# Optimization experiments

Measured on AMD Instinct MI355X. Metric: run time of the kernel, lower is better.

## Reference

```python
import jax, jax.numpy as jnp
import numpy as np

N = 100000   # nodes
E = 1600000  # edges (before self loops)
D = 128      # input_dim
H1 = 128     # hidden_dim_1
H2 = 128     # hidden_dim_2
OUT = 1      # output_dim
G = 64       # number of graphs in the batch


def setup_inputs() -> dict:
    key = jax.random.key(0)
    ks = jax.random.split(key, 11)
    x = jax.random.normal(ks[0], (N, D), dtype=jnp.float32)
    edge_index = jax.random.randint(ks[1], (2, E), 0, N, dtype=jnp.int64)
    batch = jnp.sort(jax.random.randint(ks[2], (N,), 0, G, dtype=jnp.int64))
    s = 0.05
    W1 = jax.random.normal(ks[3], (D, H1), dtype=jnp.float32) * s
    b1 = jnp.zeros((H1,), dtype=jnp.float32)
    W2 = jax.random.normal(ks[4], (H1, H2), dtype=jnp.float32) * s
    b2 = jnp.zeros((H2,), dtype=jnp.float32)
    W_iou = jax.random.normal(ks[5], (H2, OUT), dtype=jnp.float32) * s
    b_iou = jnp.zeros((OUT,), dtype=jnp.float32)
    W_iop = jax.random.normal(ks[6], (H2, OUT), dtype=jnp.float32) * s
    b_iop = jnp.zeros((OUT,), dtype=jnp.float32)
    return dict(x=x, edge_index=edge_index, batch=batch,
                W1=W1, b1=b1, W2=W2, b2=b2,
                W_iou=W_iou, b_iou=b_iou, W_iop=W_iop, b_iop=b_iop)


def reference(x, edge_index, batch, W1, b1, W2, b2, W_iou, b_iou, W_iop, b_iop):
    n = x.shape[0]
    # add_self_loops
    loops = jnp.arange(n, dtype=edge_index.dtype)
    src = jnp.concatenate([edge_index[0], loops])
    dst = jnp.concatenate([edge_index[1], loops])
    # symmetric GCN normalization: deg over target nodes
    deg = jax.ops.segment_sum(jnp.ones_like(dst, dtype=x.dtype), dst, num_segments=n)
    dinv = jnp.where(deg > 0, jax.lax.rsqrt(deg), 0.0)
    norm = dinv[src] * dinv[dst]  # [E+N]

    def gcn_conv(h, W, b):
        hw = h @ W                                  # [N, H]
        m = hw[src] * norm[:, None]                 # gather + normalize [E+N, H]
        return jax.ops.segment_sum(m, dst, num_segments=n) + b  # scatter-add

    h = jax.nn.relu(gcn_conv(x, W1, b1))
    h = jax.nn.relu(gcn_conv(h, W2, b2))
    # global_max_pool over graph ids
    pooled = jax.ops.segment_max(h, batch, num_segments=G)
    pooled = jnp.where(jnp.isfinite(pooled), pooled, 0.0)  # guard empty graphs
    iou = pooled @ W_iou + b_iou
    iop = pooled @ W_iop + b_iop
    return jnp.concatenate([iou, iop], axis=1)  # [G, 2*OUT]
```

## Files before the change

### kernel.cpp

```cpp
#include <hip/hip_runtime.h>
#include <math.h>

typedef unsigned int u32;
typedef __attribute__((ext_vector_type(8))) short short8v;
typedef __attribute__((ext_vector_type(4))) float floatx4;

__device__ inline int rfl(int v) { return __builtin_amdgcn_readfirstlane(v); }

__device__ inline float blo(u32 u) { return __uint_as_float(u << 16); }
__device__ inline float bhi(u32 u) { return __uint_as_float(u & 0xffff0000u); }
__device__ inline u32 f2b(float f) {
    u32 u = __float_as_uint(f);
    return (u + 0x7fffu + ((u >> 16) & 1u)) >> 16;
}
__device__ inline u32 pack2(float a, float b) { return f2b(a) | (f2b(b) << 16); }

__global__ void init_k(u32* gcursor, int B, int CAP, u32* pooled, int np) {
    int i = blockIdx.x * blockDim.x + threadIdx.x;
    if (i < np) pooled[i] = 0u;
    if (i < B) gcursor[i] = (u32)i * (u32)CAP;
}

__global__ __launch_bounds__(256) void wprep_k(const float* __restrict__ W1, const float* __restrict__ W2,
                                               ushort* __restrict__ W1t, ushort* __restrict__ W2t) {
    int idx = blockIdx.x * 256 + threadIdx.x;
    int k = idx >> 7, j = idx & 127;
    W1t[j * 128 + k] = (ushort)f2b(W1[idx]);
    W2t[j * 128 + k] = (ushort)f2b(W2[idx]);
}

#define FILL_EPT 16
__global__ __launch_bounds__(256) void bfill_k(const int* __restrict__ src, const int* __restrict__ dst,
                                               u32* __restrict__ gcursor, u32* __restrict__ pairs,
                                               int E, int B, int CAP) {
    __shared__ u32 lcnt[256];
    __shared__ u32 lbase[256];
    const int t = threadIdx.x;
    lcnt[t] = 0;
    __syncthreads();

    const int base_e = blockIdx.x * (256 * FILL_EPT);
    u32 pk[FILL_EPT];
    u32 bk[FILL_EPT];
    u32 rk[FILL_EPT];
#pragma unroll
    for (int j = 0; j < FILL_EPT; ++j) {
        int e = base_e + t + j * 256;
        pk[j] = 0xFFFFFFFFu;
        if (e < E) {
            int d = dst[e];
            int s = src[e];
            u32 b = (u32)d >> 9;
            pk[j] = (u32)s | (((u32)d & 511u) << 17);
            bk[j] = b;
            rk[j] = atomicAdd(&lcnt[b], 1u);
        }
    }
    __syncthreads();
    if (t < B) {
        u32 v = lcnt[t];
        lbase[t] = v ? atomicAdd(&gcursor[t], v) : 0u;
    }
    __syncthreads();
#pragma unroll
    for (int j = 0; j < FILL_EPT; ++j) {
        if (pk[j] != 0xFFFFFFFFu) {
            u32 b = bk[j];
            u32 pos = lbase[b] + rk[j];
            if (pos < (b + 1u) * (u32)CAP) pairs[pos] = pk[j];
        }
    }
}

__global__ __launch_bounds__(256) void csort_k(const u32* __restrict__ pairs, const u32* __restrict__ gcursor,
                                               u32* __restrict__ csr, uint2* __restrict__ rowinfo,
                                               float* __restrict__ dinv, int N, int CAP) {
    __shared__ u32 hist[512];
    __shared__ u32 excl[512];
    __shared__ u32 pscan[256];
    const int b = blockIdx.x, t = threadIdx.x;
    const u32 base = (u32)b * (u32)CAP;
    u32 cnt = gcursor[b] - base;
    if (cnt > (u32)CAP) cnt = (u32)CAP;

    hist[t] = 0u; hist[t + 256] = 0u;
    __syncthreads();
    for (u32 j = t; j < cnt; j += 256) {
        u32 p = pairs[base + j];
        atomicAdd(&hist[p >> 17], 1u);
    }
    __syncthreads();
    u32 a = hist[2 * t], c = hist[2 * t + 1];
    u32 s = a + c;
    pscan[t] = s;
    __syncthreads();
    for (int off = 1; off < 256; off <<= 1) {
        u32 v = (t >= off) ? pscan[t - off] : 0u;
        __syncthreads();
        pscan[t] += v;
        __syncthreads();
    }
    u32 e0 = pscan[t] - s;
    excl[2 * t] = e0;
    excl[2 * t + 1] = e0 + a;
    __syncthreads();
    const int node0 = b << 9;
#pragma unroll
    for (int q = 0; q < 2; ++q) {
        int loc = t + q * 256;
        int i = node0 + loc;
        if (i < N) {
            u32 dg = hist[loc];
            rowinfo[i] = make_uint2(base + excl[loc], dg);
            dinv[i] = rsqrtf((float)(dg + 1u));
        }
    }
    __syncthreads();
    for (u32 j = t; j < cnt; j += 256) {
        u32 p = pairs[base + j];
        u32 loc = p >> 17;
        u32 pos = atomicAdd(&excl[loc], 1u);
        csr[base + pos] = p & 0x1FFFFu;
    }
}

__device__ inline int swz(int row, int kbyte) { return row * 256 + (kbyte ^ ((row & 7) << 4)); }

template <bool BF16IN>
__global__ __launch_bounds__(256) void gemm_mfma_k(const void* __restrict__ inp, const ushort* __restrict__ Wt,
                                                   const float* __restrict__ dinv,
                                                   ushort* __restrict__ outp, int N) {
    __shared__ char Xl[128 * 256];
    __shared__ char Wl[128 * 256];
    const int t = threadIdx.x;
    const int brow = blockIdx.x * 128;

    {
        const uint4* g = (const uint4*)Wt;
#pragma unroll
        for (int i = 0; i < 8; ++i) {
            int f = t + i * 256;
            int r = f >> 4, kb = (f & 15) << 4;
            *(uint4*)(Wl + swz(r, kb)) = g[f];
        }
    }
    if (BF16IN) {
#pragma unroll
        for (int i = 0; i < 8; ++i) {
            int f = t + i * 256;
            int r = f >> 4, kb = (f & 15) << 4;
            int gr = brow + r;
            uint4 v = make_uint4(0u, 0u, 0u, 0u);
            if (gr < N) v = ((const uint4*)inp)[gr * 16 + (kb >> 4)];
            *(uint4*)(Xl + swz(r, kb)) = v;
        }
    } else {
#pragma unroll
        for (int i = 0; i < 16; ++i) {
            int f = t + i * 256;
            int r = f >> 5, c4 = (f & 31) << 2;
            int gr = brow + r;
            uint2 v = make_uint2(0u, 0u);
            if (gr < N) {
                float4 x = ((const float4*)inp)[gr * 32 + (c4 >> 2)];
                v.x = pack2(x.x, x.y);
                v.y = pack2(x.z, x.w);
            }
            *(uint2*)(Xl + swz(r, c4 * 2)) = v;
        }
    }
    __syncthreads();

    const int lane = t & 63;
    const int wave = t >> 6;
    const int l15 = lane & 15;
    const int lk = (lane >> 4) * 16;

    floatx4 acc[2][8];
#pragma unroll
    for (int mt = 0; mt < 2; ++mt)
#pragma unroll
        for (int nt = 0; nt < 8; ++nt) acc[mt][nt] = (floatx4){0.f, 0.f, 0.f, 0.f};

#pragma unroll
    for (int ks = 0; ks < 4; ++ks) {
        int kb = ks * 64 + lk;
        short8v a[2], b[8];
#pragma unroll
        for (int mt = 0; mt < 2; ++mt) {
            int row = wave * 32 + mt * 16 + l15;
            a[mt] = *(const short8v*)(Xl + swz(row, kb));
        }
#pragma unroll
        for (int nt = 0; nt < 8; ++nt) {
            int jr = nt * 16 + l15;
            b[nt] = *(const short8v*)(Wl + swz(jr, kb));
        }
#pragma unroll
        for (int mt = 0; mt < 2; ++mt)
#pragma unroll
            for (int nt = 0; nt < 8; ++nt)
                acc[mt][nt] = __builtin_amdgcn_mfma_f32_16x16x32_bf16(a[mt], b[nt], acc[mt][nt], 0, 0, 0);
    }

    const int r0w = (lane >> 4) * 4;
#pragma unroll
    for (int mt = 0; mt < 2; ++mt) {
#pragma unroll
        for (int reg = 0; reg < 4; ++reg) {
            int grow = brow + wave * 32 + mt * 16 + r0w + reg;
            if (grow < N) {
                float sc = dinv[grow];
#pragma unroll
                for (int nt = 0; nt < 8; ++nt)
                    outp[grow * 128 + nt * 16 + l15] = (ushort)f2b(acc[mt][nt][reg] * sc);
            }
        }
    }
}

__global__ __launch_bounds__(256) void edge_accum_k(const u32* __restrict__ hw, const uint2* __restrict__ rowinfo,
                                                    const u32* __restrict__ csr, const float* __restrict__ dinv,
                                                    const float* __restrict__ bias, u32* __restrict__ hout, int N) {
    const int lane = threadIdx.x & 63;
    const int wid = (blockIdx.x * blockDim.x + threadIdx.x) >> 6;
    const int nw = (gridDim.x * blockDim.x) >> 6;
    const float2 bb = ((const float2*)bias)[lane];

    for (int i = wid; i < N; i += nw) {
        uint2 ri = rowinfo[i];
        const int r0 = rfl((int)ri.x);
        const int deg = rfl((int)ri.y);
        float di = dinv[i];
        u32 us = hw[(size_t)i * 64 + lane];
        float a0 = blo(us), a1 = bhi(us);

        int j = 0;
        for (; j + 8 <= deg; j += 8) {
            int s0 = rfl((int)csr[r0 + j + 0]);
            int s1 = rfl((int)csr[r0 + j + 1]);
            int s2 = rfl((int)csr[r0 + j + 2]);
            int s3 = rfl((int)csr[r0 + j + 3]);
            int s4 = rfl((int)csr[r0 + j + 4]);
            int s5 = rfl((int)csr[r0 + j + 5]);
            int s6 = rfl((int)csr[r0 + j + 6]);
            int s7 = rfl((int)csr[r0 + j + 7]);
            u32 u0 = hw[(size_t)s0 * 64 + lane];
            u32 u1 = hw[(size_t)s1 * 64 + lane];
            u32 u2 = hw[(size_t)s2 * 64 + lane];
            u32 u3 = hw[(size_t)s3 * 64 + lane];
            u32 u4 = hw[(size_t)s4 * 64 + lane];
            u32 u5 = hw[(size_t)s5 * 64 + lane];
            u32 u6 = hw[(size_t)s6 * 64 + lane];
            u32 u7 = hw[(size_t)s7 * 64 + lane];
            a0 += blo(u0); a1 += bhi(u0);
            a0 += blo(u1); a1 += bhi(u1);
            a0 += blo(u2); a1 += bhi(u2);
            a0 += blo(u3); a1 += bhi(u3);
            a0 += blo(u4); a1 += bhi(u4);
            a0 += blo(u5); a1 += bhi(u5);
            a0 += blo(u6); a1 += bhi(u6);
            a0 += blo(u7); a1 += bhi(u7);
        }
        for (; j < deg; ++j) {
            int s = rfl((int)csr[r0 + j]);
            u32 u = hw[(size_t)s * 64 + lane];
            a0 += blo(u); a1 += bhi(u);
        }

        a0 = fmaxf(fmaf(a0, di, bb.x), 0.f);
        a1 = fmaxf(fmaf(a1, di, bb.y), 0.f);
        hout[(size_t)i * 64 + lane] = pack2(a0, a1);
    }
}

__global__ __launch_bounds__(64) void pool_k(const u32* __restrict__ h2, const int* __restrict__ batch,
                                             u32* __restrict__ pooled, int N) {
    int lane = threadIdx.x;
    int start = blockIdx.x * 64;
    int end = min(start + 64, N);
    if (start >= N) return;
    int gcur = batch[start];
    float m0 = 0.f, m1 = 0.f;
    for (int n = start; n < end; ++n) {
        int g = batch[n];
        if (g != gcur) {
            atomicMax(pooled + gcur * 128 + lane * 2, __float_as_uint(m0));
            atomicMax(pooled + gcur * 128 + lane * 2 + 1, __float_as_uint(m1));
            gcur = g;
            m0 = m1 = 0.f;
        }
        u32 u = h2[n * 64 + lane];
        m0 = fmaxf(m0, blo(u));
        m1 = fmaxf(m1, bhi(u));
    }
    atomicMax(pooled + gcur * 128 + lane * 2, __float_as_uint(m0));
    atomicMax(pooled + gcur * 128 + lane * 2 + 1, __float_as_uint(m1));
}

__global__ void final_k(const float* __restrict__ pooled, const float* __restrict__ Wu, const float* __restrict__ bu,
                        const float* __restrict__ Wp, const float* __restrict__ bp, float* __restrict__ out) {
    int t = threadIdx.x;
    int g = t >> 1, c = t & 1;
    const float* w = c ? Wp : Wu;
    const float* pr = pooled + g * 128;
    float s = 0.f;
    for (int k = 0; k < 128; k += 4)
        s += pr[k] * w[k] + pr[k + 1] * w[k + 1] + pr[k + 2] * w[k + 2] + pr[k + 3] * w[k + 3];
    out[g * 2 + c] = s + (c ? bp[0] : bu[0]);
}

extern "C" void kernel_launch(void* const* d_in, const int* in_sizes, int n_in,
                              void* d_out, int out_size, void* d_ws, size_t ws_size,
                              hipStream_t stream) {
    const float* x     = (const float*)d_in[0];
    const int*   ei    = (const int*)d_in[1];
    const int*   batch = (const int*)d_in[2];
    const float* W1    = (const float*)d_in[3];
    const float* b1    = (const float*)d_in[4];
    const float* W2    = (const float*)d_in[5];
    const float* b2    = (const float*)d_in[6];
    const float* Wu    = (const float*)d_in[7];
    const float* bu    = (const float*)d_in[8];
    const float* Wp    = (const float*)d_in[9];
    const float* bp    = (const float*)d_in[10];
    float* out = (float*)d_out;

    const int N = in_sizes[2];
    const int E = in_sizes[1] / 2;
    const int* src = ei;
    const int* dst = ei + E;

    const int B = (N + 511) >> 9;
    int avg = E / B;
    int CAP = avg + 6 * (int)sqrt((double)avg) + 64;
    CAP = (CAP + 63) & ~63;

    char* ws = (char*)d_ws;
    size_t o = 0;
    auto alloc = [&](size_t bytes) { size_t r = o; o += (bytes + 255) & ~(size_t)255; return r; };
    u32*   gcursor = (u32*)(ws + alloc(1024));
    float* dinv    = (float*)(ws + alloc((size_t)N * 4));
    uint2* rowinfo = (uint2*)(ws + alloc((size_t)N * 8));
    u32*   csr     = (u32*)(ws + alloc((size_t)B * CAP * 4));
    ushort* hwA    = (ushort*)(ws + alloc((size_t)N * 128 * 2));
    ushort* hB     = (ushort*)(ws + alloc((size_t)N * 128 * 2));
    u32*   pooled  = (u32*)(ws + alloc(64 * 128 * 4));
    ushort* W1t    = (ushort*)(ws + alloc(128 * 128 * 2));
    ushort* W2t    = (ushort*)(ws + alloc(128 * 128 * 2));
    u32*   pairs   = (u32*)hwA;
    (void)ws_size; (void)n_in;

    const int gFill = (E + 256 * FILL_EPT - 1) / (256 * FILL_EPT);
    const int gGemm = (N + 127) / 128;
    const int gPool = (N + 63) / 64;

    init_k<<<32, 256, 0, stream>>>(gcursor, B, CAP, pooled, 64 * 128);
    wprep_k<<<64, 256, 0, stream>>>(W1, W2, W1t, W2t);
    bfill_k<<<gFill, 256, 0, stream>>>(src, dst, gcursor, pairs, E, B, CAP);
    csort_k<<<B, 256, 0, stream>>>(pairs, gcursor, csr, rowinfo, dinv, N, CAP);

    gemm_mfma_k<false><<<gGemm, 256, 0, stream>>>((const void*)x, W1t, dinv, hwA, N);
    edge_accum_k<<<2048, 256, 0, stream>>>((const u32*)hwA, rowinfo, csr, dinv, b1, (u32*)hB, N);
    gemm_mfma_k<true><<<gGemm, 256, 0, stream>>>((const void*)hB, W2t, dinv, hwA, N);
    edge_accum_k<<<2048, 256, 0, stream>>>((const u32*)hwA, rowinfo, csr, dinv, b2, (u32*)hB, N);

    pool_k<<<gPool, 64, 0, stream>>>((const u32*)hB, batch, pooled, N);
    final_k<<<1, 128, 0, stream>>>((const float*)pooled, Wu, bu, Wp, bp, out);
}
```

Baseline: 246.3 us.

## Fuse layer-2 GEMM into first aggregation and pooling into second aggregation

```diff
diff --git a/kernel.cpp b/kernel.cpp
--- a/kernel.cpp
+++ b/kernel.cpp
@@ -22,11 +22,19 @@
 }
 
 __global__ __launch_bounds__(256) void wprep_k(const float* __restrict__ W1, const float* __restrict__ W2,
-                                               ushort* __restrict__ W1t, ushort* __restrict__ W2t) {
+                                               ushort* __restrict__ W1t, uint2* __restrict__ W2p) {
     int idx = blockIdx.x * 256 + threadIdx.x;
-    int k = idx >> 7, j = idx & 127;
-    W1t[j * 128 + k] = (ushort)f2b(W1[idx]);
-    W2t[j * 128 + k] = (ushort)f2b(W2[idx]);
+    if (idx < 16384) {
+        int k = idx >> 7, j = idx & 127;
+        W1t[j * 128 + k] = (ushort)f2b(W1[idx]);
+    } else if (idx < 16384 + 4096) {
+        int r = idx - 16384;
+        int m = r >> 6, L = r & 63;
+        uint2 w;
+        w.x = pack2(W2[(2 * m) * 128 + 2 * L],     W2[(2 * m) * 128 + 2 * L + 1]);
+        w.y = pack2(W2[(2 * m + 1) * 128 + 2 * L], W2[(2 * m + 1) * 128 + 2 * L + 1]);
+        W2p[r] = w;
+    }
 }
 
 #define FILL_EPT 16
@@ -126,8 +134,7 @@
 
 __device__ inline int swz(int row, int kbyte) { return row * 256 + (kbyte ^ ((row & 7) << 4)); }
 
-template <bool BF16IN>
-__global__ __launch_bounds__(256) void gemm_mfma_k(const void* __restrict__ inp, const ushort* __restrict__ Wt,
+__global__ __launch_bounds__(256) void gemm_mfma_k(const float* __restrict__ inp, const ushort* __restrict__ Wt,
                                                    const float* __restrict__ dinv,
                                                    ushort* __restrict__ outp, int N) {
     __shared__ char Xl[128 * 256];
@@ -144,30 +151,18 @@
             *(uint4*)(Wl + swz(r, kb)) = g[f];
         }
     }
-    if (BF16IN) {
-#pragma unroll
-        for (int i = 0; i < 8; ++i) {
-            int f = t + i * 256;
-            int r = f >> 4, kb = (f & 15) << 4;
-            int gr = brow + r;
-            uint4 v = make_uint4(0u, 0u, 0u, 0u);
-            if (gr < N) v = ((const uint4*)inp)[gr * 16 + (kb >> 4)];
-            *(uint4*)(Xl + swz(r, kb)) = v;
-        }
-    } else {
-#pragma unroll
-        for (int i = 0; i < 16; ++i) {
-            int f = t + i * 256;
-            int r = f >> 5, c4 = (f & 31) << 2;
-            int gr = brow + r;
-            uint2 v = make_uint2(0u, 0u);
-            if (gr < N) {
-                float4 x = ((const float4*)inp)[gr * 32 + (c4 >> 2)];
-                v.x = pack2(x.x, x.y);
-                v.y = pack2(x.z, x.w);
-            }
-            *(uint2*)(Xl + swz(r, c4 * 2)) = v;
-        }
+#pragma unroll
+    for (int i = 0; i < 16; ++i) {
+        int f = t + i * 256;
+        int r = f >> 5, c4 = (f & 31) << 2;
+        int gr = brow + r;
+        uint2 v = make_uint2(0u, 0u);
+        if (gr < N) {
+            float4 x = ((const float4*)inp)[gr * 32 + (c4 >> 2)];
+            v.x = pack2(x.x, x.y);
+            v.y = pack2(x.z, x.w);
+        }
+        *(uint2*)(Xl + swz(r, c4 * 2)) = v;
     }
     __syncthreads();
 
@@ -219,83 +214,149 @@
     }
 }
 
-__global__ __launch_bounds__(256) void edge_accum_k(const u32* __restrict__ hw, const uint2* __restrict__ rowinfo,
+template <int MODE>
+__global__ __launch_bounds__(512) void edge_fused_k(const u32* __restrict__ hw, const uint2* __restrict__ rowinfo,
                                                     const u32* __restrict__ csr, const float* __restrict__ dinv,
-                                                    const float* __restrict__ bias, u32* __restrict__ hout, int N) {
+                                                    const float* __restrict__ bias, const uint2* __restrict__ W2p,
+                                                    u32* __restrict__ outbuf, const int* __restrict__ batch,
+                                                    u32* __restrict__ pooled, int N, int chunk) {
     const int lane = threadIdx.x & 63;
-    const int wid = (blockIdx.x * blockDim.x + threadIdx.x) >> 6;
-    const int nw = (gridDim.x * blockDim.x) >> 6;
+    const int gwid = (blockIdx.x * blockDim.x + threadIdx.x) >> 6;
     const float2 bb = ((const float2*)bias)[lane];
 
-    for (int i = wid; i < N; i += nw) {
-        uint2 ri = rowinfo[i];
-        const int r0 = rfl((int)ri.x);
-        const int deg = rfl((int)ri.y);
-        float di = dinv[i];
-        u32 us = hw[(size_t)i * 64 + lane];
-        float a0 = blo(us), a1 = bhi(us);
-
-        int j = 0;
-        for (; j + 8 <= deg; j += 8) {
-            int s0 = rfl((int)csr[r0 + j + 0]);
-            int s1 = rfl((int)csr[r0 + j + 1]);
-            int s2 = rfl((int)csr[r0 + j + 2]);
-            int s3 = rfl((int)csr[r0 + j + 3]);
-            int s4 = rfl((int)csr[r0 + j + 4]);
-            int s5 = rfl((int)csr[r0 + j + 5]);
-            int s6 = rfl((int)csr[r0 + j + 6]);
-            int s7 = rfl((int)csr[r0 + j + 7]);
-            u32 u0 = hw[(size_t)s0 * 64 + lane];
-            u32 u1 = hw[(size_t)s1 * 64 + lane];
-            u32 u2 = hw[(size_t)s2 * 64 + lane];
-            u32 u3 = hw[(size_t)s3 * 64 + lane];
-            u32 u4 = hw[(size_t)s4 * 64 + lane];
-            u32 u5 = hw[(size_t)s5 * 64 + lane];
-            u32 u6 = hw[(size_t)s6 * 64 + lane];
-            u32 u7 = hw[(size_t)s7 * 64 + lane];
-            a0 += blo(u0); a1 += bhi(u0);
-            a0 += blo(u1); a1 += bhi(u1);
-            a0 += blo(u2); a1 += bhi(u2);
-            a0 += blo(u3); a1 += bhi(u3);
-            a0 += blo(u4); a1 += bhi(u4);
-            a0 += blo(u5); a1 += bhi(u5);
-            a0 += blo(u6); a1 += bhi(u6);
-            a0 += blo(u7); a1 += bhi(u7);
-        }
-        for (; j < deg; ++j) {
-            int s = rfl((int)csr[r0 + j]);
-            u32 u = hw[(size_t)s * 64 + lane];
-            a0 += blo(u); a1 += bhi(u);
-        }
-
-        a0 = fmaxf(fmaf(a0, di, bb.x), 0.f);
-        a1 = fmaxf(fmaf(a1, di, bb.y), 0.f);
-        hout[(size_t)i * 64 + lane] = pack2(a0, a1);
-    }
-}
-
-__global__ __launch_bounds__(64) void pool_k(const u32* __restrict__ h2, const int* __restrict__ batch,
-                                             u32* __restrict__ pooled, int N) {
-    int lane = threadIdx.x;
-    int start = blockIdx.x * 64;
-    int end = min(start + 64, N);
-    if (start >= N) return;
-    int gcur = batch[start];
-    float m0 = 0.f, m1 = 0.f;
-    for (int n = start; n < end; ++n) {
-        int g = batch[n];
-        if (g != gcur) {
-            atomicMax(pooled + gcur * 128 + lane * 2, __float_as_uint(m0));
+    if constexpr (MODE == 0) {
+        __shared__ uint2 W2l[64 * 64];
+        {
+            const int t = threadIdx.x;
+#pragma unroll
+            for (int q = 0; q < 8; ++q) W2l[t + q * 512] = W2p[t + q * 512];
+        }
+        __syncthreads();
+
+        int i0 = gwid * chunk, i1 = min(N, i0 + chunk);
+        for (int i = i0; i < i1; ++i) {
+            uint2 ri = rowinfo[i];
+            const int r0 = rfl((int)ri.x);
+            const int deg = rfl((int)ri.y);
+            float di = dinv[i];
+            u32 us = hw[(size_t)i * 64 + lane];
+            float a0 = blo(us), a1 = bhi(us);
+
+            int j = 0;
+            for (; j + 8 <= deg; j += 8) {
+                int s0 = rfl((int)csr[r0 + j + 0]);
+                int s1 = rfl((int)csr[r0 + j + 1]);
+                int s2 = rfl((int)csr[r0 + j + 2]);
+                int s3 = rfl((int)csr[r0 + j + 3]);
+                int s4 = rfl((int)csr[r0 + j + 4]);
+                int s5 = rfl((int)csr[r0 + j + 5]);
+                int s6 = rfl((int)csr[r0 + j + 6]);
+                int s7 = rfl((int)csr[r0 + j + 7]);
+                u32 u0 = hw[(size_t)s0 * 64 + lane];
+                u32 u1 = hw[(size_t)s1 * 64 + lane];
+                u32 u2 = hw[(size_t)s2 * 64 + lane];
+                u32 u3 = hw[(size_t)s3 * 64 + lane];
+                u32 u4 = hw[(size_t)s4 * 64 + lane];
+                u32 u5 = hw[(size_t)s5 * 64 + lane];
+                u32 u6 = hw[(size_t)s6 * 64 + lane];
+                u32 u7 = hw[(size_t)s7 * 64 + lane];
+                a0 += blo(u0); a1 += bhi(u0);
+                a0 += blo(u1); a1 += bhi(u1);
+                a0 += blo(u2); a1 += bhi(u2);
+                a0 += blo(u3); a1 += bhi(u3);
+                a0 += blo(u4); a1 += bhi(u4);
+                a0 += blo(u5); a1 += bhi(u5);
+                a0 += blo(u6); a1 += bhi(u6);
+                a0 += blo(u7); a1 += bhi(u7);
+            }
+            for (; j < deg; ++j) {
+                int s = rfl((int)csr[r0 + j]);
+                u32 u = hw[(size_t)s * 64 + lane];
+                a0 += blo(u); a1 += bhi(u);
+            }
+
+            a0 = fmaxf(fmaf(a0, di, bb.x), 0.f);
+            a1 = fmaxf(fmaf(a1, di, bb.y), 0.f);
+
+            u32 ph = pack2(a0, a1);
+            float acc0 = 0.f, acc1 = 0.f;
+#pragma unroll
+            for (int m = 0; m < 64; ++m) {
+                u32 hk = __builtin_amdgcn_readlane(ph, m);
+                float h0 = blo(hk), h1v = bhi(hk);
+                uint2 w = W2l[m * 64 + lane];
+                acc0 = fmaf(h0, blo(w.x), acc0);
+                acc1 = fmaf(h0, bhi(w.x), acc1);
+                acc0 = fmaf(h1v, blo(w.y), acc0);
+                acc1 = fmaf(h1v, bhi(w.y), acc1);
+            }
+            outbuf[(size_t)i * 64 + lane] = pack2(acc0 * di, acc1 * di);
+        }
+    } else {
+        int i0 = gwid * chunk, i1 = min(N, i0 + chunk);
+        float m0 = 0.f, m1 = 0.f;
+        int gcur = -1;
+        for (int i = i0; i < i1; ++i) {
+            uint2 ri = rowinfo[i];
+            const int r0 = rfl((int)ri.x);
+            const int deg = rfl((int)ri.y);
+            float di = dinv[i];
+            u32 us = hw[(size_t)i * 64 + lane];
+            float a0 = blo(us), a1 = bhi(us);
+
+            int j = 0;
+            for (; j + 8 <= deg; j += 8) {
+                int s0 = rfl((int)csr[r0 + j + 0]);
+                int s1 = rfl((int)csr[r0 + j + 1]);
+                int s2 = rfl((int)csr[r0 + j + 2]);
+                int s3 = rfl((int)csr[r0 + j + 3]);
+                int s4 = rfl((int)csr[r0 + j + 4]);
+                int s5 = rfl((int)csr[r0 + j + 5]);
+                int s6 = rfl((int)csr[r0 + j + 6]);
+                int s7 = rfl((int)csr[r0 + j + 7]);
+                u32 u0 = hw[(size_t)s0 * 64 + lane];
+                u32 u1 = hw[(size_t)s1 * 64 + lane];
+                u32 u2 = hw[(size_t)s2 * 64 + lane];
+                u32 u3 = hw[(size_t)s3 * 64 + lane];
+                u32 u4 = hw[(size_t)s4 * 64 + lane];
+                u32 u5 = hw[(size_t)s5 * 64 + lane];
+                u32 u6 = hw[(size_t)s6 * 64 + lane];
+                u32 u7 = hw[(size_t)s7 * 64 + lane];
+                a0 += blo(u0); a1 += bhi(u0);
+                a0 += blo(u1); a1 += bhi(u1);
+                a0 += blo(u2); a1 += bhi(u2);
+                a0 += blo(u3); a1 += bhi(u3);
+                a0 += blo(u4); a1 += bhi(u4);
+                a0 += blo(u5); a1 += bhi(u5);
+                a0 += blo(u6); a1 += bhi(u6);
+                a0 += blo(u7); a1 += bhi(u7);
+            }
+            for (; j < deg; ++j) {
+                int s = rfl((int)csr[r0 + j]);
+                u32 u = hw[(size_t)s * 64 + lane];
+                a0 += blo(u); a1 += bhi(u);
+            }
+
+            a0 = fmaxf(fmaf(a0, di, bb.x), 0.f);
+            a1 = fmaxf(fmaf(a1, di, bb.y), 0.f);
+
+            int g = batch[i];
+            if (g != gcur) {
+                if (gcur >= 0) {
+                    atomicMax(pooled + gcur * 128 + lane * 2,     __float_as_uint(m0));
+                    atomicMax(pooled + gcur * 128 + lane * 2 + 1, __float_as_uint(m1));
+                }
+                gcur = g;
+                m0 = m1 = 0.f;
+            }
+            m0 = fmaxf(m0, a0);
+            m1 = fmaxf(m1, a1);
+        }
+        if (gcur >= 0) {
+            atomicMax(pooled + gcur * 128 + lane * 2,     __float_as_uint(m0));
             atomicMax(pooled + gcur * 128 + lane * 2 + 1, __float_as_uint(m1));
-            gcur = g;
-            m0 = m1 = 0.f;
-        }
-        u32 u = h2[n * 64 + lane];
-        m0 = fmaxf(m0, blo(u));
-        m1 = fmaxf(m1, bhi(u));
-    }
-    atomicMax(pooled + gcur * 128 + lane * 2, __float_as_uint(m0));
-    atomicMax(pooled + gcur * 128 + lane * 2 + 1, __float_as_uint(m1));
+        }
+    }
 }
 
 __global__ void final_k(const float* __restrict__ pooled, const float* __restrict__ Wu, const float* __restrict__ bu,
@@ -344,27 +405,28 @@
     uint2* rowinfo = (uint2*)(ws + alloc((size_t)N * 8));
     u32*   csr     = (u32*)(ws + alloc((size_t)B * CAP * 4));
     ushort* hwA    = (ushort*)(ws + alloc((size_t)N * 128 * 2));
-    ushort* hB     = (ushort*)(ws + alloc((size_t)N * 128 * 2));
+    ushort* hwB    = (ushort*)(ws + alloc((size_t)N * 128 * 2));
     u32*   pooled  = (u32*)(ws + alloc(64 * 128 * 4));
     ushort* W1t    = (ushort*)(ws + alloc(128 * 128 * 2));
-    ushort* W2t    = (ushort*)(ws + alloc(128 * 128 * 2));
+    uint2* W2p     = (uint2*)(ws + alloc(64 * 64 * 8));
     u32*   pairs   = (u32*)hwA;
     (void)ws_size; (void)n_in;
 
     const int gFill = (E + 256 * FILL_EPT - 1) / (256 * FILL_EPT);
     const int gGemm = (N + 127) / 128;
-    const int gPool = (N + 63) / 64;
+    const int nWaves = 1024 * 8;
+    const int chunk = (N + nWaves - 1) / nWaves;
 
     init_k<<<32, 256, 0, stream>>>(gcursor, B, CAP, pooled, 64 * 128);
-    wprep_k<<<64, 256, 0, stream>>>(W1, W2, W1t, W2t);
+    wprep_k<<<80, 256, 0, stream>>>(W1, W2, W1t, W2p);
     bfill_k<<<gFill, 256, 0, stream>>>(src, dst, gcursor, pairs, E, B, CAP);
     csort_k<<<B, 256, 0, stream>>>(pairs, gcursor, csr, rowinfo, dinv, N, CAP);
 
-    gemm_mfma_k<false><<<gGemm, 256, 0, stream>>>((const void*)x, W1t, dinv, hwA, N);
-    edge_accum_k<<<2048, 256, 0, stream>>>((const u32*)hwA, rowinfo, csr, dinv, b1, (u32*)hB, N);
-    gemm_mfma_k<true><<<gGemm, 256, 0, stream>>>((const void*)hB, W2t, dinv, hwA, N);
-    edge_accum_k<<<2048, 256, 0, stream>>>((const u32*)hwA, rowinfo, csr, dinv, b2, (u32*)hB, N);
-
-    pool_k<<<gPool, 64, 0, stream>>>((const u32*)hB, batch, pooled, N);
+    gemm_mfma_k<<<gGemm, 256, 0, stream>>>(x, W1t, dinv, hwA, N);
+    edge_fused_k<0><<<1024, 512, 0, stream>>>((const u32*)hwA, rowinfo, csr, dinv, b1, W2p,
+                                              (u32*)hwB, batch, pooled, N, chunk);
+    edge_fused_k<1><<<1024, 512, 0, stream>>>((const u32*)hwB, rowinfo, csr, dinv, b2, W2p,
+                                              nullptr, batch, pooled, N, chunk);
+
     final_k<<<1, 128, 0, stream>>>((const float*)pooled, Wu, bu, Wp, bp, out);
 }
```

After: 487.7 us. 1.98x slower.
